# Kernel optimization log

Measured on AMD Instinct MI355X. Metric: run time of the kernel, lower is better.

The kernel has to match this reference:

```python
import jax, jax.numpy as jnp
import numpy as np

# FP4 E2M1 constants (from the torch module)
EXP_BITS = 2
EXP_BIAS = 1          # 2**(EXP_BITS-1) - 1
MANT_BITS = 1
MAX_EXP_FIELD = 3     # (1 << EXP_BITS) - 1
MIN_NORMAL_EXP = 0    # 1 - EXP_BIAS
FP4_MAX = 6.0         # (1 + 1/2) * 2**(MAX_EXP_FIELD-1 - EXP_BIAS + 1) = 1.5 * 4
GROUP = 128


def fp4_quant_dequant(x):
    """Faithful composition of _float_to_fp4 followed by _fp4_to_float (E2M1,
    subnormal-aware), expressed in float arithmetic (bit pack/unpack cancels)."""
    a = jnp.abs(x)
    zero_mask = a == 0
    a_safe = jnp.where(zero_mask, jnp.float32(1e-8), a)
    e = jnp.floor(jnp.log2(a_safe))                      # unbiased exponent
    is_sub = e < MIN_NORMAL_EXP
    e_c = jnp.clip(e, MIN_NORMAL_EXP, MAX_EXP_FIELD - EXP_BIAS)
    mant_scale = float(1 << MANT_BITS)                   # 2.0
    mant_normal = jnp.clip(jnp.round((a_safe / jnp.exp2(e_c) - 1.0) * mant_scale), 0.0, mant_scale - 1.0)
    mant_sub = jnp.clip(jnp.round(a_safe / (2.0 ** MIN_NORMAL_EXP) * mant_scale), 0.0, mant_scale - 1.0)
    mant = jnp.where(is_sub, mant_sub, mant_normal)
    # decode (_fp4_to_float): normals (1 + m/2)*2^(e), subnormals (m/2)*2^(1-bias)
    val_normal = (1.0 + mant / mant_scale) * jnp.exp2(e_c)
    val_sub = (mant / mant_scale) * (2.0 ** (1 - EXP_BIAS))
    val = jnp.where(is_sub, val_sub, val_normal)
    val = jnp.where(x < 0, -val, val)
    return jnp.where(zero_mask, jnp.zeros_like(val), val)


def setup_inputs() -> dict:
    key = jax.random.key(0)
    k1, k2, k3 = jax.random.split(key, 3)
    x = jax.random.normal(k1, (4096, 4096), dtype=jnp.float32)
    weight = jax.random.normal(k2, (4096, 4096), dtype=jnp.float32) * 0.02
    b = jax.random.normal(k3, (4096,), dtype=jnp.float32)
    return {"x": x, "weight": weight, "b": b}


def reference(x, weight, b):
    out_f, in_f = weight.shape
    wg = weight.reshape(out_f, in_f // GROUP, GROUP)
    amax = jnp.max(jnp.abs(wg), axis=-1, keepdims=True)       # [out, groups, 1]
    scale = jnp.where(amax == 0, jnp.float32(1.0), amax / FP4_MAX)
    w_deq = (fp4_quant_dequant(wg / scale) * scale).reshape(out_f, in_f)
    return x @ w_deq.T + b
```

## Files before the change

### kernel.cpp

```cpp
#include <hip/hip_runtime.h>
#include <hip/hip_bf16.h>
#include <stdint.h>

#define KDIM 4096
#define NDIM 4096
#define MDIM 4096
#define BM 256
#define BN 256
#define BK 64

typedef __attribute__((ext_vector_type(8))) short bf16x8;
typedef __attribute__((ext_vector_type(4))) float f32x4;


__device__ __forceinline__ unsigned short bf16bits(float f) {
    union { float f; uint32_t u; } c; c.f = f;
    uint32_t u = c.u;
    uint32_t r = (u + 0x7fffu + ((u >> 16) & 1u)) >> 16;
    return (unsigned short)r;
}

__device__ __forceinline__ float fp4qd(float x) {
    float a = fabsf(x);
    if (a == 0.0f) return 0.0f;
    float e = floorf(log2f(a));
    float val;
    if (e < 0.0f) {
        float mant = fminf(fmaxf(rintf(a * 2.0f), 0.0f), 1.0f);
        val = mant * 0.5f;
    } else {
        float ec = fminf(e, 2.0f);
        float p  = exp2f(ec);
        float mant = fminf(fmaxf(rintf((a / p - 1.0f) * 2.0f), 0.0f), 1.0f);
        val = (1.0f + 0.5f * mant) * p;
    }
    return (x < 0.0f) ? -val : val;
}

__device__ __forceinline__ void gld16(void* lds, const void* g) {
    __builtin_amdgcn_global_load_lds(
        (const __attribute__((address_space(1))) unsigned int*)g,
        (__attribute__((address_space(3))) unsigned int*)lds,
        16, 0, 0);
}

__global__ __launch_bounds__(256) void prep_kernel(const float* __restrict__ X,
                                                   const float* __restrict__ W,
                                                   unsigned short* __restrict__ Xb,
                                                   unsigned short* __restrict__ Wq) {
    int bid = blockIdx.x;
    int tid = threadIdx.x;
    if (bid < 16384) {
        size_t i = ((size_t)bid * 256 + tid) * 4;
        float4 v = *(const float4*)(X + i);
        ushort4 o;
        o.x = bf16bits(v.x); o.y = bf16bits(v.y);
        o.z = bf16bits(v.z); o.w = bf16bits(v.w);
        *(ushort4*)(Xb + i) = o;
    } else {
        size_t base = ((size_t)(bid - 16384) * 256 + tid) * 4;
        float4 v = *(const float4*)(W + base);
        float am = fmaxf(fmaxf(fabsf(v.x), fabsf(v.y)),
                         fmaxf(fabsf(v.z), fabsf(v.w)));
        #pragma unroll
        for (int s = 16; s; s >>= 1) am = fmaxf(am, __shfl_xor(am, s));
        float scale = (am == 0.0f) ? 1.0f : am / 6.0f;
        ushort4 o;
        o.x = bf16bits(fp4qd(v.x / scale) * scale);
        o.y = bf16bits(fp4qd(v.y / scale) * scale);
        o.z = bf16bits(fp4qd(v.z / scale) * scale);
        o.w = bf16bits(fp4qd(v.w / scale) * scale);
        *(ushort4*)(Wq + base) = o;
    }
}


#define BAR()    __builtin_amdgcn_s_barrier()
#define LGKM0()  asm volatile("s_waitcnt lgkmcnt(0)" ::: "memory")
#define VM4()    asm volatile("s_waitcnt vmcnt(4)" ::: "memory")
#define SCH0()   __builtin_amdgcn_sched_barrier(0)
#define PRIO(x)  __builtin_amdgcn_s_setprio(x)

__global__ __launch_bounds__(512, 2) void gemm256(const unsigned short* __restrict__ A,
                                                  const unsigned short* __restrict__ B,
                                                  const float* __restrict__ bias,
                                                  float* __restrict__ C) {
    __shared__ __attribute__((aligned(16))) char smem[2][2][2][16384];
    char* sm = (char*)&smem[0][0][0][0];

    const int t = threadIdx.x;
    const int l = t & 63;
    const int w = __builtin_amdgcn_readfirstlane(t >> 6);
    const int wm = w >> 2;
    const int wn = w & 3;

    int bid = blockIdx.x;
    int swz = (bid & 7) * 32 + (bid >> 3);
    int brow = (swz >> 4) * BM;
    int bcol = (swz & 15) * BN;

    const int lr8  = l >> 3;
    const int slot = l & 7;
    const int scol = (slot ^ lr8) << 3;
    const unsigned short* pA = A + (size_t)(brow + w * 8 + lr8) * KDIM + scol;
    const unsigned short* pB = B + (size_t)(bcol + w * 8 + lr8) * KDIM + scol;

#define STAGE(b, op, h, kt) do {                                               \
    const unsigned short* _s = ((op) ? pB : pA)                                \
        + (size_t)(h) * 128 * KDIM + (size_t)(kt) * BK;                        \
    gld16(sm + (b) * 65536 + (op) * 32768 + (h) * 16384 + w * 1024, _s);       \
    gld16(sm + (b) * 65536 + (op) * 32768 + (h) * 16384 + 8192 + w * 1024,     \
          _s + (size_t)64 * KDIM);                                             \
} while (0)

    const int fr  = l & 15;
    const int fq  = l >> 4;
    const int kx0 = ((fq    ) ^ (fr & 7)) << 4;
    const int kx1 = ((fq + 4) ^ (fr & 7)) << 4;
    const int frA = fr * 128;

#define RD_A(b, mh) do {                                                        \
    const char* _p = sm + (b) * 65536 + wm * 16384 + (mh) * 8192 + frA;         \
    _Pragma("unroll")                                                           \
    for (int m = 0; m < 4; ++m) {                                               \
        av[m][0] = *(const bf16x8*)(_p + m * 2048 + kx0);                       \
        av[m][1] = *(const bf16x8*)(_p + m * 2048 + kx1);                       \
    }                                                                           \
} while (0)

#define RD_B(b, nh, arr) do {                                                   \
    const char* _p = sm + (b) * 65536 + 32768 + wn * 8192 + (nh) * 4096 + frA;  \
    _Pragma("unroll")                                                           \
    for (int n = 0; n < 2; ++n) {                                               \
        arr[n][0] = *(const bf16x8*)(_p + n * 2048 + kx0);                      \
        arr[n][1] = *(const bf16x8*)(_p + n * 2048 + kx1);                      \
    }                                                                           \
} while (0)

#define MM(mh, nh, B_)                                                          \
    _Pragma("unroll")                                                           \
    for (int ks = 0; ks < 2; ++ks)                                              \
        _Pragma("unroll")                                                       \
        for (int m = 0; m < 4; ++m)                                             \
            _Pragma("unroll")                                                   \
            for (int n = 0; n < 2; ++n)                                         \
                acc[(mh) * 4 + m][(nh) * 2 + n] =                               \
                    __builtin_amdgcn_mfma_f32_16x16x32_bf16(                    \
                        av[m][ks], B_[n][ks], acc[(mh) * 4 + m][(nh) * 2 + n],  \
                        0, 0, 0);

    f32x4 acc[8][4];
    #pragma unroll
    for (int m = 0; m < 8; ++m)
        #pragma unroll
        for (int n = 0; n < 4; ++n)
            acc[m][n] = f32x4{0.f, 0.f, 0.f, 0.f};

    bf16x8 av[4][2], bvA[2][2], bvB[2][2];

    STAGE(0, 0, 0, 0); STAGE(0, 0, 1, 0); STAGE(0, 1, 0, 0); STAGE(0, 1, 1, 0);
    STAGE(1, 1, 0, 1); STAGE(1, 0, 0, 1);
    VM4();
    BAR();
    RD_B(0, 0, bvA);
    SCH0();

    for (int it = 0; it < 32; ++it) {
        const int k1 = 2 * it + 1;
        const int k2 = (2 * it + 2) & 63;
        const int k3 = (2 * it + 3) & 63;

        RD_A(0, 0); RD_B(0, 1, bvB);
        STAGE(1, 0, 1, k1); STAGE(1, 1, 1, k1);
        BAR(); LGKM0(); SCH0();
        PRIO(1); MM(0, 0, bvA); MM(0, 1, bvB); PRIO(0);
        RD_A(0, 1);
        STAGE(0, 1, 0, k2); STAGE(0, 0, 0, k2);
        BAR(); LGKM0(); SCH0();
        PRIO(1); MM(1, 1, bvB); MM(1, 0, bvA); PRIO(0);
        VM4(); RD_B(1, 0, bvA);

        RD_A(1, 0); RD_B(1, 1, bvB);
        STAGE(0, 0, 1, k2); STAGE(0, 1, 1, k2);
        BAR(); LGKM0(); SCH0();
        PRIO(1); MM(0, 0, bvA); MM(0, 1, bvB); PRIO(0);
        RD_A(1, 1);
        STAGE(1, 1, 0, k3); STAGE(1, 0, 0, k3);
        BAR(); LGKM0(); SCH0();
        PRIO(1); MM(1, 1, bvB); MM(1, 0, bvA); PRIO(0);
        VM4(); RD_B(0, 0, bvA);
    }

    float bb[4];
    #pragma unroll
    for (int n = 0; n < 4; ++n) bb[n] = bias[bcol + wn * 64 + n * 16 + fr];
    #pragma unroll
    for (int mi = 0; mi < 8; ++mi) {
        #pragma unroll
        for (int q = 0; q < 4; ++q) {
            int row = brow + wm * 128 + mi * 16 + fq * 4 + q;
            float* crow = C + (size_t)row * NDIM + bcol + wn * 64;
            #pragma unroll
            for (int n = 0; n < 4; ++n)
                crow[n * 16 + fr] = acc[mi][n][q] + bb[n];
        }
    }
}

extern "C" void kernel_launch(void* const* d_in, const int* in_sizes, int n_in,
                              void* d_out, int out_size, void* d_ws, size_t ws_size,
                              hipStream_t stream) {
    const float* x = (const float*)d_in[0];
    const float* w = (const float*)d_in[1];
    const float* b = (const float*)d_in[2];
    float* out = (float*)d_out;

    unsigned short* xb = (unsigned short*)d_ws;
    unsigned short* wq = xb + (size_t)NDIM * KDIM;

    prep_kernel<<<32768, 256, 0, stream>>>(x, w, xb, wq);
    gemm256<<<(MDIM / BM) * (NDIM / BN), 512, 0, stream>>>(xb, wq, b, out);
}
```

Before: 148.6 us.

## Restructure GEMM main loop into full-tile double buffering with one barrier

The GEMM main loop becomes one macro per K-tile. It first issues all global→LDS loads for the next tile into the other buffer, then runs the MFMAs for both M halves. After that it waits for vmcnt(0), takes a single barrier, and preloads every A and B fragment for the next tile into registers. This replaces the old schedule of four barriers per two tiles, with its partial vmcnt(4) waits and interleaved half-tile stages. The aim is fewer barrier stalls and more overlap of LDS reads with MFMAs. In exchange it holds two full sets of A fragments in registers, which raises VGPR pressure under the 512x2 launch bound and risks spills.

```diff
diff --git a/kernel.cpp b/kernel.cpp
--- a/kernel.cpp
+++ b/kernel.cpp
@@ -76,8 +76,8 @@
 
 
 #define BAR()    __builtin_amdgcn_s_barrier()
-#define LGKM0()  asm volatile("s_waitcnt lgkmcnt(0)" ::: "memory")
-#define VM4()    asm volatile("s_waitcnt vmcnt(4)" ::: "memory")
+#define LGKM(n)  asm volatile("s_waitcnt lgkmcnt(" #n ")" ::: "memory")
+#define VM0()    asm volatile("s_waitcnt vmcnt(0)" ::: "memory")
 #define SCH0()   __builtin_amdgcn_sched_barrier(0)
 #define PRIO(x)  __builtin_amdgcn_s_setprio(x)
 
@@ -119,12 +119,12 @@
     const int kx1 = ((fq + 4) ^ (fr & 7)) << 4;
     const int frA = fr * 128;
 
-#define RD_A(b, mh) do {                                                        \
+#define RD_A(b, mh, arr) do {                                                   \
     const char* _p = sm + (b) * 65536 + wm * 16384 + (mh) * 8192 + frA;         \
     _Pragma("unroll")                                                           \
     for (int m = 0; m < 4; ++m) {                                               \
-        av[m][0] = *(const bf16x8*)(_p + m * 2048 + kx0);                       \
-        av[m][1] = *(const bf16x8*)(_p + m * 2048 + kx1);                       \
+        arr[m][0] = *(const bf16x8*)(_p + m * 2048 + kx0);                      \
+        arr[m][1] = *(const bf16x8*)(_p + m * 2048 + kx1);                      \
     }                                                                           \
 } while (0)
 
@@ -137,17 +137,20 @@
     }                                                                           \
 } while (0)
 
-#define MM(mh, nh, B_)                                                          \
+#define MMG(mh, AV)                                                             \
     _Pragma("unroll")                                                           \
     for (int ks = 0; ks < 2; ++ks)                                              \
         _Pragma("unroll")                                                       \
-        for (int m = 0; m < 4; ++m)                                             \
-            _Pragma("unroll")                                                   \
-            for (int n = 0; n < 2; ++n)                                         \
-                acc[(mh) * 4 + m][(nh) * 2 + n] =                               \
-                    __builtin_amdgcn_mfma_f32_16x16x32_bf16(                    \
-                        av[m][ks], B_[n][ks], acc[(mh) * 4 + m][(nh) * 2 + n],  \
-                        0, 0, 0);
+        for (int m = 0; m < 4; ++m) {                                           \
+            acc[(mh)*4+m][0] = __builtin_amdgcn_mfma_f32_16x16x32_bf16(         \
+                AV[m][ks], bvA[0][ks], acc[(mh)*4+m][0], 0, 0, 0);              \
+            acc[(mh)*4+m][1] = __builtin_amdgcn_mfma_f32_16x16x32_bf16(         \
+                AV[m][ks], bvA[1][ks], acc[(mh)*4+m][1], 0, 0, 0);              \
+            acc[(mh)*4+m][2] = __builtin_amdgcn_mfma_f32_16x16x32_bf16(         \
+                AV[m][ks], bvB[0][ks], acc[(mh)*4+m][2], 0, 0, 0);              \
+            acc[(mh)*4+m][3] = __builtin_amdgcn_mfma_f32_16x16x32_bf16(         \
+                AV[m][ks], bvB[1][ks], acc[(mh)*4+m][3], 0, 0, 0);              \
+        }
 
     f32x4 acc[8][4];
     #pragma unroll
@@ -156,39 +159,32 @@
         for (int n = 0; n < 4; ++n)
             acc[m][n] = f32x4{0.f, 0.f, 0.f, 0.f};
 
-    bf16x8 av[4][2], bvA[2][2], bvB[2][2];
+    bf16x8 avE[4][2], avO[4][2], bvA[2][2], bvB[2][2];
+
+#define TILE_K(b, ktNext) do {                                                  \
+    STAGE((b)^1, 0, 0, ktNext); STAGE((b)^1, 0, 1, ktNext);                     \
+    STAGE((b)^1, 1, 0, ktNext); STAGE((b)^1, 1, 1, ktNext);                     \
+    LGKM(8); SCH0();                                                            \
+    PRIO(1); MMG(0, avE); PRIO(0);                                              \
+    LGKM(0); SCH0();                                                            \
+    VM0();                                                                      \
+    BAR(); SCH0();                                                              \
+    PRIO(1); MMG(1, avO); PRIO(0);                                              \
+    RD_B((b)^1, 0, bvA); RD_B((b)^1, 1, bvB);                                   \
+    RD_A((b)^1, 0, avE); RD_A((b)^1, 1, avO);                                   \
+} while (0)
 
     STAGE(0, 0, 0, 0); STAGE(0, 0, 1, 0); STAGE(0, 1, 0, 0); STAGE(0, 1, 1, 0);
-    STAGE(1, 1, 0, 1); STAGE(1, 0, 0, 1);
-    VM4();
-    BAR();
-    RD_B(0, 0, bvA);
-    SCH0();
+    VM0();
+    BAR(); SCH0();
+    RD_B(0, 0, bvA); RD_B(0, 1, bvB);
+    RD_A(0, 0, avE); RD_A(0, 1, avO);
 
     for (int it = 0; it < 32; ++it) {
         const int k1 = 2 * it + 1;
         const int k2 = (2 * it + 2) & 63;
-        const int k3 = (2 * it + 3) & 63;
-
-        RD_A(0, 0); RD_B(0, 1, bvB);
-        STAGE(1, 0, 1, k1); STAGE(1, 1, 1, k1);
-        BAR(); LGKM0(); SCH0();
-        PRIO(1); MM(0, 0, bvA); MM(0, 1, bvB); PRIO(0);
-        RD_A(0, 1);
-        STAGE(0, 1, 0, k2); STAGE(0, 0, 0, k2);
-        BAR(); LGKM0(); SCH0();
-        PRIO(1); MM(1, 1, bvB); MM(1, 0, bvA); PRIO(0);
-        VM4(); RD_B(1, 0, bvA);
-
-        RD_A(1, 0); RD_B(1, 1, bvB);
-        STAGE(0, 0, 1, k2); STAGE(0, 1, 1, k2);
-        BAR(); LGKM0(); SCH0();
-        PRIO(1); MM(0, 0, bvA); MM(0, 1, bvB); PRIO(0);
-        RD_A(1, 1);
-        STAGE(1, 1, 0, k3); STAGE(1, 0, 0, k3);
-        BAR(); LGKM0(); SCH0();
-        PRIO(1); MM(1, 1, bvB); MM(1, 0, bvA); PRIO(0);
-        VM4(); RD_B(0, 0, bvA);
+        TILE_K(0, k1);
+        TILE_K(1, k2);
     }
 
     float bb[4];
```

Result: no change. 149.9 us (+0.9%).
